# Kernel tuning notes

Hardware: AMD Instinct MI355X
Metric: run time of the kernel (lower is better)

## Reference

```python
import jax, jax.numpy as jnp
import numpy as np

B, IN_DIM, C, E, TOPK = 16384, 768, 50, 8, 2
RH = 256          # router hidden_dim
HS = [512, 256]   # expert hidden_sizes
THR = 0.05        # BitNet-1.58b ternarization threshold


def _xavier(k, shape):
    fan_out, fan_in = shape[-2], shape[-1]
    lim = float(np.sqrt(6.0 / (fan_in + fan_out)))
    return jax.random.uniform(k, shape, jnp.float32, -lim, lim)


def setup_inputs() -> dict:
    key = jax.random.key(0)
    ks = jax.random.split(key, 8)
    return {
        "x": jax.random.normal(ks[0], (B, IN_DIM), jnp.float32),
        # Router MLP: in_dim -> RH -> RH//2 -> E (torch Linear: W is (out,in))
        "rW1": _xavier(ks[1], (RH, IN_DIM)), "rb1": jnp.zeros((RH,), jnp.float32),
        "rW2": _xavier(ks[2], (RH // 2, RH)), "rb2": jnp.zeros((RH // 2,), jnp.float32),
        "rW3": _xavier(ks[3], (E, RH // 2)), "rb3": jnp.zeros((E,), jnp.float32),
        # Stacked expert weights: (E, out, in)
        "eW1": _xavier(ks[4], (E, HS[0], IN_DIM)), "eb1": jnp.zeros((E, HS[0]), jnp.float32),
        "eW2": _xavier(ks[5], (E, HS[1], HS[0])), "eb2": jnp.zeros((E, HS[1]), jnp.float32),
        "eW3": _xavier(ks[6], (E, C, HS[1])), "eb3": jnp.zeros((E, C), jnp.float32),
    }


def _ternary(W):
    # BitNet-1.58b: ternarize weights with |w|>threshold, scale by mean |W| per matrix
    scale = jnp.mean(jnp.abs(W), axis=(-2, -1), keepdims=True)
    Wq = jnp.sign(W) * (jnp.abs(W) > THR).astype(W.dtype)
    return Wq * scale


def reference(x, rW1, rb1, rW2, rb2, rW3, rb3, eW1, eb1, eW2, eb2, eW3, eb3):
    # ---- Router (eval mode: dropout = identity) ----
    h = jax.nn.relu(x @ rW1.T + rb1)
    h = jax.nn.relu(h @ rW2.T + rb2)
    router_logits = h @ rW3.T + rb3                      # (B, E)
    router_p = jax.nn.softmax(router_logits, axis=1)     # (B, E)

    # ---- Top-k gating; scatter gate weights back to dense (B, E) ----
    k_val, k_idx = jax.lax.top_k(router_p, TOPK)         # (B, K)
    rows = jnp.arange(x.shape[0])[:, None]
    gate = jnp.zeros_like(router_p).at[rows, k_idx].set(k_val)  # 0 for unselected experts

    # ---- Batched ternary-quantized expert MLPs (all experts, all samples) ----
    W1q, W2q, W3q = _ternary(eW1), _ternary(eW2), _ternary(eW3)
    a1 = jax.nn.relu(jnp.einsum('bd,ehd->ebh', x, W1q) + eb1[:, None, :])   # (E,B,H1)
    a2 = jax.nn.relu(jnp.einsum('ebh,egh->ebg', a1, W2q) + eb2[:, None, :]) # (E,B,H2)
    expert_logits = jnp.einsum('ebg,ecg->ebc', a2, W3q) + eb3[:, None, :]   # (E,B,C)

    # ---- Weighted combine over top-k experts (equivalent to the per-expert loop) ----
    out = jnp.einsum('ebc,be->bc', expert_logits, gate) / TOPK              # (B,C)

    lb_loss = jnp.float32(0.0)  # eval mode: self.training is False
    return (out, router_p, lb_loss)
```

## Files before the change

kernel.cpp:

```cpp
#include <hip/hip_runtime.h>
#include <hip/hip_bf16.h>

typedef __attribute__((ext_vector_type(4))) float f32x4;
typedef __attribute__((ext_vector_type(8))) short bf16x8;

#define B_ROWS 16384
#define IN_DIM 768
#define H1 512
#define H2 256
#define NC 50
#define NE 8
#define RH1 256
#define RH2 128
#define CHK 128

static __device__ __forceinline__ f32x4 mfma16(bf16x8 a, bf16x8 b, f32x4 c) {
    return __builtin_amdgcn_mfma_f32_16x16x32_bf16(a, b, c, 0, 0, 0);
}

static __device__ __forceinline__ bf16x8 expand_frag(uint2 pw) {
    unsigned q0 = (pw.x & 0x01010101u) << 7;
    unsigned q1 = (pw.y & 0x01010101u) << 7;
    union { unsigned u[4]; bf16x8 v; } r;
    r.u[0] = __builtin_amdgcn_perm(pw.x, q0, 0x05010400u);
    r.u[1] = __builtin_amdgcn_perm(pw.x, q0, 0x07030602u);
    r.u[2] = __builtin_amdgcn_perm(pw.y, q1, 0x05010400u);
    r.u[3] = __builtin_amdgcn_perm(pw.y, q1, 0x07030602u);
    return r.v;
}

static __device__ __forceinline__ void decomp_f4(float4 v, ushort4* hv, ushort4* lv) {
    float vv[4] = {v.x, v.y, v.z, v.w};
    ushort ho[4], lo4[4];
    #pragma unroll
    for (int q = 0; q < 4; ++q) {
        __hip_bfloat16 h = __float2bfloat16(vv[q]);
        float hf = __bfloat162float(h);
        __hip_bfloat16 l = __float2bfloat16(vv[q] - hf);
        ho[q] = *(ushort*)&h; lo4[q] = *(ushort*)&l;
    }
    *hv = make_ushort4(ho[0], ho[1], ho[2], ho[3]);
    *lv = make_ushort4(lo4[0], lo4[1], lo4[2], lo4[3]);
}

__global__ __launch_bounds__(512) void pack_absum_kernel(
    const float* __restrict__ eW1, const float* __restrict__ eW2, const float* __restrict__ eW3,
    unsigned char* __restrict__ W1p8, unsigned char* __restrict__ W2p8,
    unsigned char* __restrict__ W3p8,
    float* __restrict__ p1, float* __restrict__ p2, float* __restrict__ p3,
    const float* __restrict__ rW1, ushort* __restrict__ rw1hp, ushort* __restrict__ rw1lp,
    const float* __restrict__ rW2, ushort* __restrict__ rw2hp, ushort* __restrict__ rw2lp,
    int* __restrict__ counts)
{
    if (blockIdx.y == 24) {
        int u = blockIdx.x * 512 + threadIdx.x;
        const float* src; ushort* dh; ushort* dl;
        if (u < 24576) {
            int lane = u & 63, nblk = (u >> 6) & 15, ks = u >> 10;
            int n = nblk * 16 + (lane & 15), k = ks * 32 + (lane >> 4) * 8;
            src = rW1 + (size_t)n * IN_DIM + k;
            dh = rw1hp + (size_t)u * 8; dl = rw1lp + (size_t)u * 8;
        } else {
            int v = u - 24576;
            if (v >= 4096) return;
            int lane = v & 63, nblk = (v >> 6) & 7, ks = v >> 9;
            int n = nblk * 16 + (lane & 15), k = ks * 32 + (lane >> 4) * 8;
            src = rW2 + (size_t)n * RH1 + k;
            dh = rw2hp + (size_t)v * 8; dl = rw2lp + (size_t)v * 8;
        }
        ushort oh[8], ol[8];
        #pragma unroll
        for (int j = 0; j < 8; ++j) {
            float w = src[j];
            __hip_bfloat16 h = __float2bfloat16(w);
            float hf = __bfloat162float(h);
            __hip_bfloat16 l = __float2bfloat16(w - hf);
            oh[j] = *(ushort*)&h; ol[j] = *(ushort*)&l;
        }
        ((ushort4*)dh)[0] = make_ushort4(oh[0], oh[1], oh[2], oh[3]);
        ((ushort4*)dh)[1] = make_ushort4(oh[4], oh[5], oh[6], oh[7]);
        ((ushort4*)dl)[0] = make_ushort4(ol[0], ol[1], ol[2], ol[3]);
        ((ushort4*)dl)[1] = make_ushort4(ol[4], ol[5], ol[6], ol[7]);
        return;
    }

    const int mat = blockIdx.y >> 3, e = blockIdx.y & 7;
    const int u = blockIdx.x * 512 + threadIdx.x;
    if (blockIdx.x == 0 && blockIdx.y == 0 && threadIdx.x < 8) counts[threadIdx.x] = 0;
    const float* src; unsigned char* dst; int valid = 1; float* P; int np;
    if (mat == 0) {
        int lane = u & 63, nblk = (u >> 6) & 31, ks = u >> 11;
        int n = nblk * 16 + (lane & 15), k = ks * 32 + (lane >> 4) * 8;
        src = eW1 + ((size_t)e * H1 + n) * IN_DIM + k;
        dst = W1p8 + (size_t)e * 393216
            + (size_t)ks * 16384 + (nblk >> 1) * 1024 + lane * 16 + (nblk & 1) * 8;
        P = p1; np = 96;
    } else if (mat == 1) {
        int lane = u & 63, nblk = (u >> 6) & 15, ks = u >> 10;
        if (u >= 16384) {
            float s = 0.f;
            const int lane2 = threadIdx.x & 63, wave2 = threadIdx.x >> 6;
            #pragma unroll
            for (int o = 32; o; o >>= 1) s += __shfl_down(s, o);
            __shared__ float redp[8];
            if (lane2 == 0) redp[wave2] = s;
            __syncthreads();
            return;
        }
        int n = nblk * 16 + (lane & 15), k = ks * 32 + (lane >> 4) * 8;
        src = eW2 + ((size_t)e * H2 + n) * H1 + k;
        dst = W2p8 + (size_t)e * 131072
            + (size_t)ks * 8192 + (nblk >> 1) * 1024 + lane * 16 + (nblk & 1) * 8;
        P = p2; np = 32;
    } else {
        if (u >= 2048) {
            float s = 0.f;
            const int lane2 = threadIdx.x & 63, wave2 = threadIdx.x >> 6;
            #pragma unroll
            for (int o = 32; o; o >>= 1) s += __shfl_down(s, o);
            __shared__ float redp2[8];
            if (lane2 == 0) redp2[wave2] = s;
            __syncthreads();
            return;
        }
        int lane = u & 63, nblk = (u >> 6) & 3, ks = u >> 8;
        int n = nblk * 16 + (lane & 15), k = ks * 32 + (lane >> 4) * 8;
        valid = (n < NC);
        src = eW3 + ((size_t)e * NC + (valid ? n : 0)) * H2 + k;
        dst = W3p8 + ((size_t)e * 2048 + u) * 8;
        P = p3; np = 4;
    }
    unsigned lo = 0, hi = 0;
    float s = 0.f;
    #pragma unroll
    for (int j = 0; j < 4; ++j) {
        float w = valid ? src[j] : 0.f;
        s += fabsf(w);
        unsigned c = (fabsf(w) > 0.05f) ? (w > 0.f ? 0x3Fu : 0xBFu) : 0u;
        lo |= c << (8 * j);
    }
    #pragma unroll
    for (int j = 0; j < 4; ++j) {
        float w = valid ? src[4 + j] : 0.f;
        s += fabsf(w);
        unsigned c = (fabsf(w) > 0.05f) ? (w > 0.f ? 0x3Fu : 0xBFu) : 0u;
        hi |= c << (8 * j);
    }
    *(uint2*)dst = make_uint2(lo, hi);
    const int lane = threadIdx.x & 63, wave = threadIdx.x >> 6;
    #pragma unroll
    for (int o = 32; o; o >>= 1) s += __shfl_down(s, o);
    __shared__ float red[8];
    if (lane == 0) red[wave] = s;
    __syncthreads();
    if (threadIdx.x == 0) {
        float t = 0.f;
        #pragma unroll
        for (int i = 0; i < 8; ++i) t += red[i];
        P[e * np + blockIdx.x] = t;
    }
}

__global__ __launch_bounds__(1024) void router_fused_kernel(
    const float* __restrict__ x, ushort* __restrict__ xh_out,
    const ushort* __restrict__ rw1hp, const ushort* __restrict__ rw1lp, const float* __restrict__ rb1,
    const ushort* __restrict__ rw2hp, const ushort* __restrict__ rw2lp, const float* __restrict__ rb2,
    const float* __restrict__ rW3, const float* __restrict__ rb3,
    float* __restrict__ router_p, float* __restrict__ gate,
    float* __restrict__ lb_out, int* __restrict__ t2)
{
    __shared__ __align__(16) unsigned char smem[68608];
    ushort (*Xdh)[32][136] = (ushort(*)[32][136])(smem);
    ushort (*Xdl)[32][136] = (ushort(*)[32][136])(smem + 17408);
    ushort (*h1hs)[264]    = (ushort(*)[264])(smem + 34816);
    ushort (*h1ls)[264]    = (ushort(*)[264])(smem + 51712);
    float (*h2s)[132]      = (float(*)[132])(smem);

    const int tid = threadIdx.x, wave = tid >> 6, lane = tid & 63;
    const int lm = lane & 15, lk = lane >> 4;
    const int r0 = blockIdx.x * 32;

    const int srow = tid >> 5;
    const int sc4r = (tid & 31) * 4;
    const float* sg = x + (size_t)(r0 + srow) * IN_DIM + sc4r;
    ushort* xo = xh_out + (size_t)(r0 + srow) * IN_DIM + sc4r;

    {
        float4 sv = *(const float4*)sg;
        ushort4 hv, lv;
        decomp_f4(sv, &hv, &lv);
        *(ushort4*)&Xdh[0][srow][sc4r] = hv;
        *(ushort4*)&Xdl[0][srow][sc4r] = lv;
        *(ushort4*)xo = hv;
    }
    __syncthreads();

    {
        f32x4 acc[2] = {};
        const ushort* wph = rw1hp + (size_t)(wave * 64 + lane) * 8;
        const ushort* wpl = rw1lp + (size_t)(wave * 64 + lane) * 8;
        uint4 ph[4], pl[4];
        #pragma unroll
        for (int k = 0; k < 4; ++k) {
            ph[k] = *(const uint4*)(wph + (size_t)k * 8192);
            pl[k] = *(const uint4*)(wpl + (size_t)k * 8192);
        }
        for (int i = 0; i < 6; ++i) {
            float4 sv;
            if (i + 1 < 6) sv = *(const float4*)(sg + (i + 1) * CHK);
            const ushort (*Xch)[136] = Xdh[i & 1];
            const ushort (*Xcl)[136] = Xdl[i & 1];
            #pragma unroll
            for (int k4 = 0; k4 < 4; ++k4) {
                uint4 ch = ph[k4], cl = pl[k4];
                if (i + 1 < 6) {
                    ph[k4] = *(const uint4*)(wph + (size_t)(4 * i + 4 + k4) * 8192);
                    pl[k4] = *(const uint4*)(wpl + (size_t)(4 * i + 4 + k4) * 8192);
                }
                const int ko = k4 * 32 + lk * 8;
                bf16x8 ah0 = *(const bf16x8*)&Xch[lm][ko];
                bf16x8 al0 = *(const bf16x8*)&Xcl[lm][ko];
                bf16x8 ah1 = *(const bf16x8*)&Xch[16 + lm][ko];
                bf16x8 al1 = *(const bf16x8*)&Xcl[16 + lm][ko];
                bf16x8 bh = *(bf16x8*)&ch;
                bf16x8 bl = *(bf16x8*)&cl;
                acc[0] = mfma16(ah0, bh, acc[0]);
                acc[0] = mfma16(ah0, bl, acc[0]);
                acc[0] = mfma16(al0, bh, acc[0]);
                acc[1] = mfma16(ah1, bh, acc[1]);
                acc[1] = mfma16(ah1, bl, acc[1]);
                acc[1] = mfma16(al1, bh, acc[1]);
            }
            if (i + 1 < 6) {
                ushort4 hv, lv;
                decomp_f4(sv, &hv, &lv);
                *(ushort4*)&Xdh[(i + 1) & 1][srow][sc4r] = hv;
                *(ushort4*)&Xdl[(i + 1) & 1][srow][sc4r] = lv;
                *(ushort4*)(xo + (i + 1) * CHK) = hv;
            }
            __syncthreads();
        }
        int col = wave * 16 + lm;
        float bv = rb1[col];
        #pragma unroll
        for (int m = 0; m < 2; ++m)
            #pragma unroll
            for (int r = 0; r < 4; ++r) {
                float v = acc[m][r] + bv;
                v = v > 0.f ? v : 0.f;
                __hip_bfloat16 h = __float2bfloat16(v);
                float hf = __bfloat162float(h);
                __hip_bfloat16 l = __float2bfloat16(v - hf);
                int row = m * 16 + lk * 4 + r;
                h1hs[row][col] = *(ushort*)&h;
                h1ls[row][col] = *(ushort*)&l;
            }
    }
    __syncthreads();

    {
        const int mt = wave >> 3, nb = wave & 7;
        const ushort* w2h = rw2hp + (size_t)(nb * 64 + lane) * 8;
        const ushort* w2l = rw2lp + (size_t)(nb * 64 + lane) * 8;
        f32x4 acc2 = {};
        uint4 pha = *(const uint4*)(w2h);
        uint4 pla = *(const uint4*)(w2l);
        uint4 phb = *(const uint4*)(w2h + 4096);
        uint4 plb = *(const uint4*)(w2l + 4096);
        for (int s = 0; s < 8; s += 2) {
            uint4 cha = pha, cla = pla, chb = phb, clb = plb;
            if (s + 2 < 8) {
                pha = *(const uint4*)(w2h + (size_t)(s + 2) * 4096);
                pla = *(const uint4*)(w2l + (size_t)(s + 2) * 4096);
                phb = *(const uint4*)(w2h + (size_t)(s + 3) * 4096);
                plb = *(const uint4*)(w2l + (size_t)(s + 3) * 4096);
            }
            {
                const int ko = s * 32 + lk * 8;
                bf16x8 ah = *(const bf16x8*)&h1hs[mt * 16 + lm][ko];
                bf16x8 al = *(const bf16x8*)&h1ls[mt * 16 + lm][ko];
                bf16x8 bh = *(bf16x8*)&cha;
                bf16x8 bl = *(bf16x8*)&cla;
                acc2 = mfma16(ah, bh, acc2);
                acc2 = mfma16(ah, bl, acc2);
                acc2 = mfma16(al, bh, acc2);
            }
            {
                const int ko = (s + 1) * 32 + lk * 8;
                bf16x8 ah = *(const bf16x8*)&h1hs[mt * 16 + lm][ko];
                bf16x8 al = *(const bf16x8*)&h1ls[mt * 16 + lm][ko];
                bf16x8 bh = *(bf16x8*)&chb;
                bf16x8 bl = *(bf16x8*)&clb;
                acc2 = mfma16(ah, bh, acc2);
                acc2 = mfma16(ah, bl, acc2);
                acc2 = mfma16(al, bh, acc2);
            }
        }
        __syncthreads();
        int col2 = nb * 16 + lm;
        float bv = rb2[col2];
        #pragma unroll
        for (int r = 0; r < 4; ++r) {
            float v = acc2[r] + bv;
            h2s[mt * 16 + lk * 4 + r][col2] = v > 0.f ? v : 0.f;
        }
    }
    __syncthreads();

    const int o = lane >> 3, kq = lane & 7;
    #pragma unroll
    for (int i = 0; i < 2; ++i) {
        int rloc = wave * 2 + i;
        int b = r0 + rloc;
        float s = 0.f;
        #pragma unroll
        for (int q = 0; q < 4; ++q) {
            float4 hv = *(const float4*)&h2s[rloc][kq * 16 + q * 4];
            float4 wv = *(const float4*)&rW3[o * RH2 + kq * 16 + q * 4];
            s += hv.x * wv.x + hv.y * wv.y + hv.z * wv.z + hv.w * wv.w;
        }
        s += __shfl_xor(s, 1);
        s += __shfl_xor(s, 2);
        s += __shfl_xor(s, 4);
        float logit = s + rb3[o];
        float l[8];
        #pragma unroll
        for (int j = 0; j < 8; ++j) l[j] = __shfl(logit, j * 8);
        float m = l[0];
        #pragma unroll
        for (int j = 1; j < 8; ++j) m = fmaxf(m, l[j]);
        float p[8]; float sum = 0.f;
        #pragma unroll
        for (int j = 0; j < 8; ++j) { p[j] = expf(l[j] - m); sum += p[j]; }
        float inv = 1.f / sum;
        #pragma unroll
        for (int j = 0; j < 8; ++j) p[j] *= inv;
        int i1 = 0; float v1 = p[0];
        #pragma unroll
        for (int j = 1; j < 8; ++j) if (p[j] > v1) { v1 = p[j]; i1 = j; }
        int i2 = -1; float v2 = -1.f;
        #pragma unroll
        for (int j = 0; j < 8; ++j) if (j != i1 && p[j] > v2) { v2 = p[j]; i2 = j; }
        if (lane < 8) {
            router_p[(size_t)b * 8 + lane] = p[lane];
            float gv = (lane == i1) ? v1 * 0.5f : ((lane == i2) ? v2 * 0.5f : 0.f);
            gate[(size_t)b * 8 + lane] = gv;
        }
        if (lane == 0) t2[b] = i1 | (i2 << 8);
    }
    if (blockIdx.x == 0 && tid == 0) lb_out[0] = 0.f;
}

__global__ __launch_bounds__(256) void build_lists_kernel(
    const int* __restrict__ t2, int* __restrict__ counts, int* __restrict__ ent,
    const float* __restrict__ p1, const float* __restrict__ p2, const float* __restrict__ p3,
    float* __restrict__ s1, float* __restrict__ s2, float* __restrict__ s3)
{
    if (blockIdx.x == 0 && threadIdx.x < 24) {
        int t = threadIdx.x;
        if (t < 8) {
            float a = 0.f;
            for (int i = 0; i < 96; ++i) a += p1[t * 96 + i];
            s1[t] = a / (float)(H1 * IN_DIM);
        } else if (t < 16) {
            int e = t - 8; float a = 0.f;
            for (int i = 0; i < 32; ++i) a += p2[e * 32 + i];
            s2[e] = a / (float)(H2 * H1);
        } else {
            int e = t - 16; float a = 0.f;
            for (int i = 0; i < 4; ++i) a += p3[e * 4 + i];
            s3[e] = a / (float)(NC * H2);
        }
    }
    __shared__ int hist[8], base[8];
    const int r = blockIdx.x * 256 + threadIdx.x;
    if (threadIdx.x < 8) hist[threadIdx.x] = 0;
    __syncthreads();
    const int v = t2[r];
    const int i1 = v & 255, i2 = v >> 8;
    const int rk1 = atomicAdd(&hist[i1], 1);
    const int rk2 = atomicAdd(&hist[i2], 1);
    __syncthreads();
    if (threadIdx.x < 8) base[threadIdx.x] = atomicAdd(&counts[threadIdx.x], hist[threadIdx.x]);
    __syncthreads();
    ent[i1 * B_ROWS + base[i1] + rk1] = (r << 1);
    ent[i2 * B_ROWS + base[i2] + rk2] = (r << 1) | 1;
}

__global__ __launch_bounds__(1024) void expert_fused_kernel(
    const ushort* __restrict__ xh,
    const unsigned char* __restrict__ W1p8, const unsigned char* __restrict__ W2p8,
    const unsigned char* __restrict__ W3p8,
    const float* __restrict__ s1, const float* __restrict__ s2, const float* __restrict__ s3,
    const float* __restrict__ eb1, const float* __restrict__ eb2, const float* __restrict__ eb3,
    const float* __restrict__ gate,
    const int* __restrict__ counts, const int* __restrict__ ent,
    float* __restrict__ S0, float* __restrict__ S1)
{
    int pfx[9]; pfx[0] = 0;
    #pragma unroll
    for (int i = 0; i < 8; ++i) pfx[i + 1] = pfx[i] + ((counts[i] + 63) >> 6);
    const int T = pfx[8];
    const int R = (T + 7) >> 3;
    const int xcd = blockIdx.x & 7, j = blockIdx.x >> 3;
    if (j >= R) return;
    const int g = xcd * R + j;
    if (g >= T) return;
    int e = 0;
    #pragma unroll
    for (int i = 0; i < 7; ++i) if (g >= pfx[i + 1]) e = i + 1;
    const int t = g - pfx[e];
    const int cnt = counts[e];

    __shared__ __align__(16) unsigned char smem[101376];
    __hip_bfloat16 (*A1s)[520] = (__hip_bfloat16(*)[520])(smem);
    __hip_bfloat16 (*A2s)[264] = (__hip_bfloat16(*)[264])(smem + 66560);
    ushort (*Xd)[64][136]      = (ushort(*)[64][136])(smem + 66560);
    __shared__ int rowL[64];
    __shared__ int slotL[64];
    __shared__ float gL[64];

    const int tid = threadIdx.x;
    const int wave = tid >> 6;
    const int lane = tid & 63;
    const int lm = lane & 15;
    const int lk = lane >> 4;

    if (tid < 64) {
        int idx = t * 64 + tid;
        if (idx < cnt) {
            int entv = ent[e * B_ROWS + idx];
            int r = entv >> 1;
            rowL[tid] = r;
            slotL[tid] = entv & 1;
            gL[tid] = gate[(size_t)r * NE + e];
        } else {
            rowL[tid] = -1; slotL[tid] = 0; gL[tid] = 0.f;
        }
    }
    __syncthreads();

    const int srow = tid >> 4;
    const int sc8  = (tid & 15) * 8;
    int SR = rowL[srow]; if (SR < 0) SR = 0;
    const ushort* sg = xh + (size_t)SR * IN_DIM + sc8;
    const unsigned char* Wsrc1 = W1p8 + (size_t)e * 393216;
    const unsigned char* Wsrc2 = W2p8 + (size_t)e * 131072;
    const unsigned char* Wsrc3 = W3p8 + (size_t)e * 16384;

    {
        bf16x8 sv = *(const bf16x8*)sg;
        *(bf16x8*)&Xd[0][srow][sc8] = sv;
    }
    __syncthreads();

    {
        f32x4 acc[4][2] = {};
        const int w2 = wave * 2;
        const unsigned char* wp1 = Wsrc1 + wave * 1024 + lane * 16;
        uint4 pw[4];
        #pragma unroll
        for (int k = 0; k < 4; ++k)
            pw[k] = *(const uint4*)(wp1 + (size_t)k * 16384);
        for (int i = 0; i < 6; ++i) {
            bf16x8 sv;
            if (i + 1 < 6) sv = *(const bf16x8*)(sg + (i + 1) * CHK);
            uint4 cur[4];
            #pragma unroll
            for (int k = 0; k < 4; ++k) cur[k] = pw[k];
            if (i + 1 < 6) {
                #pragma unroll
                for (int k = 0; k < 4; ++k)
                    pw[k] = *(const uint4*)(wp1 + (size_t)(4 * i + 4 + k) * 16384);
            }
            const ushort (*Xc)[136] = Xd[i & 1];
            #pragma unroll
            for (int k4 = 0; k4 < 4; ++k4) {
                const int ko = k4 * 32 + lk * 8;
                bf16x8 a0 = *(const bf16x8*)&Xc[     lm][ko];
                bf16x8 a1 = *(const bf16x8*)&Xc[16 + lm][ko];
                bf16x8 a2 = *(const bf16x8*)&Xc[32 + lm][ko];
                bf16x8 a3 = *(const bf16x8*)&Xc[48 + lm][ko];
                bf16x8 b0 = expand_frag(make_uint2(cur[k4].x, cur[k4].y));
                bf16x8 b1 = expand_frag(make_uint2(cur[k4].z, cur[k4].w));
                acc[0][0] = mfma16(a0, b0, acc[0][0]);
                acc[1][0] = mfma16(a1, b0, acc[1][0]);
                acc[2][0] = mfma16(a2, b0, acc[2][0]);
                acc[3][0] = mfma16(a3, b0, acc[3][0]);
                acc[0][1] = mfma16(a0, b1, acc[0][1]);
                acc[1][1] = mfma16(a1, b1, acc[1][1]);
                acc[2][1] = mfma16(a2, b1, acc[2][1]);
                acc[3][1] = mfma16(a3, b1, acc[3][1]);
            }
            if (i + 1 < 6) *(bf16x8*)&Xd[(i + 1) & 1][srow][sc8] = sv;
            __syncthreads();
        }
        const float* bias = eb1 + e * H1;
        const float sc = s1[e];
        #pragma unroll
        for (int n = 0; n < 2; ++n) {
            int ncol = (w2 + n) * 16 + lm;
            float bv = bias[ncol];
            #pragma unroll
            for (int m = 0; m < 4; ++m)
                #pragma unroll
                for (int r = 0; r < 4; ++r) {
                    float v = fmaf(acc[m][n][r], sc, bv);
                    v = v > 0.f ? v : 0.f;
                    A1s[m * 16 + lk * 4 + r][ncol] = __float2bfloat16(v);
                }
        }
    }
    __syncthreads();

    {
        const int mt = wave >> 3, ntw = wave & 7;
        const unsigned char* wp2 = Wsrc2 + ntw * 1024 + lane * 16;
        f32x4 acc[2][2] = {};
        uint4 pwa = *(const uint4*)(wp2);
        uint4 pwb = *(const uint4*)(wp2 + 8192);
        for (int s = 0; s < 16; s += 2) {
            uint4 c0 = pwa, c1 = pwb;
            if (s + 2 < 16) {
                pwa = *(const uint4*)(wp2 + (size_t)(s + 2) * 8192);
                pwb = *(const uint4*)(wp2 + (size_t)(s + 3) * 8192);
            }
            {
                const int ko = s * 32 + lk * 8;
                bf16x8 a0 = *(const bf16x8*)&A1s[mt * 32 +      lm][ko];
                bf16x8 a1 = *(const bf16x8*)&A1s[mt * 32 + 16 + lm][ko];
                bf16x8 b0 = expand_frag(make_uint2(c0.x, c0.y));
                bf16x8 b1 = expand_frag(make_uint2(c0.z, c0.w));
                acc[0][0] = mfma16(a0, b0, acc[0][0]);
                acc[1][0] = mfma16(a1, b0, acc[1][0]);
                acc[0][1] = mfma16(a0, b1, acc[0][1]);
                acc[1][1] = mfma16(a1, b1, acc[1][1]);
            }
            {
                const int ko = (s + 1) * 32 + lk * 8;
                bf16x8 a0 = *(const bf16x8*)&A1s[mt * 32 +      lm][ko];
                bf16x8 a1 = *(const bf16x8*)&A1s[mt * 32 + 16 + lm][ko];
                bf16x8 b0 = expand_frag(make_uint2(c1.x, c1.y));
                bf16x8 b1 = expand_frag(make_uint2(c1.z, c1.w));
                acc[0][0] = mfma16(a0, b0, acc[0][0]);
                acc[1][0] = mfma16(a1, b0, acc[1][0]);
                acc[0][1] = mfma16(a0, b1, acc[0][1]);
                acc[1][1] = mfma16(a1, b1, acc[1][1]);
            }
        }
        const float* bias = eb2 + e * H2;
        const float sc = s2[e];
        #pragma unroll
        for (int n = 0; n < 2; ++n) {
            int ncol = (ntw * 2 + n) * 16 + lm;
            float bv = bias[ncol];
            #pragma unroll
            for (int m = 0; m < 2; ++m)
                #pragma unroll
                for (int r = 0; r < 4; ++r) {
                    float v = fmaf(acc[m][n][r], sc, bv);
                    v = v > 0.f ? v : 0.f;
                    A2s[mt * 32 + m * 16 + lk * 4 + r][ncol] = __float2bfloat16(v);
                }
        }
    }
    __syncthreads();

    {
        const int mt = wave & 3, nt = wave >> 2;
        f32x4 acc = {};
        #pragma unroll
        for (int s = 0; s < 8; ++s) {
            bf16x8 a = *(const bf16x8*)&A2s[mt * 16 + lm][s * 32 + lk * 8];
            uint2 pw = *(const uint2*)(Wsrc3 + ((s * 4 + nt) * 64 + lane) * 8);
            bf16x8 b = expand_frag(pw);
            acc = mfma16(a, b, acc);
        }
        int col = nt * 16 + lm;
        if (col < NC) {
            const float bv = eb3[e * NC + col];
            const float sc = s3[e];
            #pragma unroll
            for (int r = 0; r < 4; ++r) {
                int row = mt * 16 + lk * 4 + r;
                int R2 = rowL[row];
                if (R2 >= 0) {
                    float v = gL[row] * fmaf(acc[r], sc, bv);
                    float* Sb = slotL[row] ? S1 : S0;
                    Sb[(size_t)R2 * 64 + col] = v;
                }
            }
        }
    }
}

__global__ __launch_bounds__(256) void combine_kernel(
    const float* __restrict__ S0, const float* __restrict__ S1, float* __restrict__ out)
{
    int i = blockIdx.x * 256 + threadIdx.x;
    if (i < B_ROWS * NC) {
        int row = i / NC, col = i % NC;
        out[i] = S0[(size_t)row * 64 + col] + S1[(size_t)row * 64 + col];
    }
}

extern "C" void kernel_launch(void* const* d_in, const int* in_sizes, int n_in,
                              void* d_out, int out_size, void* d_ws, size_t ws_size,
                              hipStream_t stream) {
    const float* x   = (const float*)d_in[0];
    const float* rW1 = (const float*)d_in[1];
    const float* rb1 = (const float*)d_in[2];
    const float* rW2 = (const float*)d_in[3];
    const float* rb2 = (const float*)d_in[4];
    const float* rW3 = (const float*)d_in[5];
    const float* rb3 = (const float*)d_in[6];
    const float* eW1 = (const float*)d_in[7];
    const float* eb1 = (const float*)d_in[8];
    const float* eW2 = (const float*)d_in[9];
    const float* eb2 = (const float*)d_in[10];
    const float* eW3 = (const float*)d_in[11];
    const float* eb3 = (const float*)d_in[12];

    float* out_main = (float*)d_out;
    float* router_p = out_main + (size_t)B_ROWS * NC;
    float* lb_out   = router_p + (size_t)B_ROWS * NE;

    char* ws = (char*)d_ws;
    size_t off = 0;
    unsigned char* W1p8 = (unsigned char*)(ws + off); off += (size_t)NE * 49152 * 8;
    unsigned char* W2p8 = (unsigned char*)(ws + off); off += (size_t)NE * 16384 * 8;
    unsigned char* W3p8 = (unsigned char*)(ws + off); off += (size_t)NE * 2048 * 8;
    ushort* xh  = (ushort*)(ws + off); off += (size_t)B_ROWS * IN_DIM * 2;
    float* S0   = (float*)(ws + off);  off += (size_t)B_ROWS * 64 * 4;
    float* S1   = (float*)(ws + off);  off += (size_t)B_ROWS * 64 * 4;
    ushort* rw1hp = (ushort*)(ws + off); off += (size_t)24576 * 8 * 2;
    ushort* rw1lp = (ushort*)(ws + off); off += (size_t)24576 * 8 * 2;
    ushort* rw2hp = (ushort*)(ws + off); off += (size_t)4096 * 8 * 2;
    ushort* rw2lp = (ushort*)(ws + off); off += (size_t)4096 * 8 * 2;
    float* gate = (float*)(ws + off);  off += (size_t)B_ROWS * NE * 4;
    int*   ent  = (int*)(ws + off);    off += (size_t)NE * B_ROWS * 4;
    int*   t2   = (int*)(ws + off);    off += (size_t)B_ROWS * 4;
    int* counts = (int*)(ws + off);    off += 256;
    float* s1   = (float*)(ws + off);  off += 256;
    float* s2   = (float*)(ws + off);  off += 256;
    float* s3   = (float*)(ws + off);  off += 256;
    float* p1   = (float*)(ws + off);  off += NE * 96 * 4;
    float* p2   = (float*)(ws + off);  off += NE * 32 * 4;
    float* p3   = (float*)(ws + off);  off += NE * 4 * 4;

    pack_absum_kernel<<<dim3(96, 25), 512, 0, stream>>>(
        eW1, eW2, eW3, W1p8, W2p8, W3p8, p1, p2, p3,
        rW1, rw1hp, rw1lp, rW2, rw2hp, rw2lp, counts);

    router_fused_kernel<<<B_ROWS / 32, 1024, 0, stream>>>(
        x, xh, rw1hp, rw1lp, rb1, rw2hp, rw2lp, rb2, rW3, rb3, router_p, gate, lb_out, t2);
    build_lists_kernel<<<B_ROWS / 256, 256, 0, stream>>>(
        t2, counts, ent, p1, p2, p3, s1, s2, s3);

    expert_fused_kernel<<<1024, 1024, 0, stream>>>(
        xh, W1p8, W2p8, W3p8, s1, s2, s3, eb1, eb2, eb3, gate, counts, ent, S0, S1);
    combine_kernel<<<(B_ROWS * NC + 255) / 256, 256, 0, stream>>>(S0, S1, out_main);
}
```

Before: 119.1 us.

## Retile expert GEMM warp tiles and fuse combine via atomic adds

Layer 1 switches each wave from a 64x32 tile to a 32x64 tile, and layer 2 from 32x32 to 16x64. This changes the balance between A reads from shared memory and ternary B-fragment expansion per MFMA. The two per-slot scratch buffers and the combine kernel are removed: the layer-3 results are atomically added straight into the output, which is zeroed by a memset first. This drops one kernel launch and the round trip through the scratch buffers, at the cost of float atomics, and the sum order of the two experts is no longer fixed.

```diff
diff --git a/kernel.cpp b/kernel.cpp
--- a/kernel.cpp
+++ b/kernel.cpp
@@ -395,7 +395,7 @@
     const float* __restrict__ eb1, const float* __restrict__ eb2, const float* __restrict__ eb3,
     const float* __restrict__ gate,
     const int* __restrict__ counts, const int* __restrict__ ent,
-    float* __restrict__ S0, float* __restrict__ S1)
+    float* __restrict__ out)
 {
     int pfx[9]; pfx[0] = 0;
     #pragma unroll
@@ -455,104 +455,56 @@
     __syncthreads();
 
     {
-        f32x4 acc[4][2] = {};
-        const int w2 = wave * 2;
-        const unsigned char* wp1 = Wsrc1 + wave * 1024 + lane * 16;
-        uint4 pw[4];
-        #pragma unroll
-        for (int k = 0; k < 4; ++k)
-            pw[k] = *(const uint4*)(wp1 + (size_t)k * 16384);
+        f32x4 acc[2][4] = {};
+        const int mt2 = wave >> 3;
+        const int nb4 = wave & 7;
+        const unsigned char* wp1 = Wsrc1 + nb4 * 2048 + lane * 16;
+        uint4 pw[4][2];
+        #pragma unroll
+        for (int k = 0; k < 4; ++k) {
+            pw[k][0] = *(const uint4*)(wp1 + (size_t)k * 16384);
+            pw[k][1] = *(const uint4*)(wp1 + (size_t)k * 16384 + 1024);
+        }
         for (int i = 0; i < 6; ++i) {
             bf16x8 sv;
             if (i + 1 < 6) sv = *(const bf16x8*)(sg + (i + 1) * CHK);
-            uint4 cur[4];
-            #pragma unroll
-            for (int k = 0; k < 4; ++k) cur[k] = pw[k];
+            uint4 cur[4][2];
+            #pragma unroll
+            for (int k = 0; k < 4; ++k) { cur[k][0] = pw[k][0]; cur[k][1] = pw[k][1]; }
             if (i + 1 < 6) {
                 #pragma unroll
-                for (int k = 0; k < 4; ++k)
-                    pw[k] = *(const uint4*)(wp1 + (size_t)(4 * i + 4 + k) * 16384);
+                for (int k = 0; k < 4; ++k) {
+                    pw[k][0] = *(const uint4*)(wp1 + (size_t)(4 * i + 4 + k) * 16384);
+                    pw[k][1] = *(const uint4*)(wp1 + (size_t)(4 * i + 4 + k) * 16384 + 1024);
+                }
             }
             const ushort (*Xc)[136] = Xd[i & 1];
             #pragma unroll
             for (int k4 = 0; k4 < 4; ++k4) {
                 const int ko = k4 * 32 + lk * 8;
-                bf16x8 a0 = *(const bf16x8*)&Xc[     lm][ko];
-                bf16x8 a1 = *(const bf16x8*)&Xc[16 + lm][ko];
-                bf16x8 a2 = *(const bf16x8*)&Xc[32 + lm][ko];
-                bf16x8 a3 = *(const bf16x8*)&Xc[48 + lm][ko];
-                bf16x8 b0 = expand_frag(make_uint2(cur[k4].x, cur[k4].y));
-                bf16x8 b1 = expand_frag(make_uint2(cur[k4].z, cur[k4].w));
-                acc[0][0] = mfma16(a0, b0, acc[0][0]);
-                acc[1][0] = mfma16(a1, b0, acc[1][0]);
-                acc[2][0] = mfma16(a2, b0, acc[2][0]);
-                acc[3][0] = mfma16(a3, b0, acc[3][0]);
-                acc[0][1] = mfma16(a0, b1, acc[0][1]);
-                acc[1][1] = mfma16(a1, b1, acc[1][1]);
-                acc[2][1] = mfma16(a2, b1, acc[2][1]);
-                acc[3][1] = mfma16(a3, b1, acc[3][1]);
-            }
-            if (i + 1 < 6) *(bf16x8*)&Xd[(i + 1) & 1][srow][sc8] = sv;
-            __syncthreads();
-        }
-        const float* bias = eb1 + e * H1;
-        const float sc = s1[e];
-        #pragma unroll
-        for (int n = 0; n < 2; ++n) {
-            int ncol = (w2 + n) * 16 + lm;
-            float bv = bias[ncol];
-            #pragma unroll
-            for (int m = 0; m < 4; ++m)
-                #pragma unroll
-                for (int r = 0; r < 4; ++r) {
-                    float v = fmaf(acc[m][n][r], sc, bv);
-                    v = v > 0.f ? v : 0.f;
-                    A1s[m * 16 + lk * 4 + r][ncol] = __float2bfloat16(v);
-                }
-        }
-    }
-    __syncthreads();
-
-    {
-        const int mt = wave >> 3, ntw = wave & 7;
-        const unsigned char* wp2 = Wsrc2 + ntw * 1024 + lane * 16;
-        f32x4 acc[2][2] = {};
-        uint4 pwa = *(const uint4*)(wp2);
-        uint4 pwb = *(const uint4*)(wp2 + 8192);
-        for (int s = 0; s < 16; s += 2) {
-            uint4 c0 = pwa, c1 = pwb;
-            if (s + 2 < 16) {
-                pwa = *(const uint4*)(wp2 + (size_t)(s + 2) * 8192);
-                pwb = *(const uint4*)(wp2 + (size_t)(s + 3) * 8192);
-            }
-            {
-                const int ko = s * 32 + lk * 8;
-                bf16x8 a0 = *(const bf16x8*)&A1s[mt * 32 +      lm][ko];
-                bf16x8 a1 = *(const bf16x8*)&A1s[mt * 32 + 16 + lm][ko];
-                bf16x8 b0 = expand_frag(make_uint2(c0.x, c0.y));
-                bf16x8 b1 = expand_frag(make_uint2(c0.z, c0.w));
+                bf16x8 a0 = *(const bf16x8*)&Xc[mt2 * 32 +      lm][ko];
+                bf16x8 a1 = *(const bf16x8*)&Xc[mt2 * 32 + 16 + lm][ko];
+                bf16x8 b0 = expand_frag(make_uint2(cur[k4][0].x, cur[k4][0].y));
+                bf16x8 b1 = expand_frag(make_uint2(cur[k4][0].z, cur[k4][0].w));
+                bf16x8 b2 = expand_frag(make_uint2(cur[k4][1].x, cur[k4][1].y));
+                bf16x8 b3 = expand_frag(make_uint2(cur[k4][1].z, cur[k4][1].w));
                 acc[0][0] = mfma16(a0, b0, acc[0][0]);
                 acc[1][0] = mfma16(a1, b0, acc[1][0]);
                 acc[0][1] = mfma16(a0, b1, acc[0][1]);
                 acc[1][1] = mfma16(a1, b1, acc[1][1]);
-            }
-            {
-                const int ko = (s + 1) * 32 + lk * 8;
-                bf16x8 a0 = *(const bf16x8*)&A1s[mt * 32 +      lm][ko];
-                bf16x8 a1 = *(const bf16x8*)&A1s[mt * 32 + 16 + lm][ko];
-                bf16x8 b0 = expand_frag(make_uint2(c1.x, c1.y));
-                bf16x8 b1 = expand_frag(make_uint2(c1.z, c1.w));
-                acc[0][0] = mfma16(a0, b0, acc[0][0]);
-                acc[1][0] = mfma16(a1, b0, acc[1][0]);
-                acc[0][1] = mfma16(a0, b1, acc[0][1]);
-                acc[1][1] = mfma16(a1, b1, acc[1][1]);
-            }
-        }
-        const float* bias = eb2 + e * H2;
-        const float sc = s2[e];
-        #pragma unroll
-        for (int n = 0; n < 2; ++n) {
-            int ncol = (ntw * 2 + n) * 16 + lm;
+                acc[0][2] = mfma16(a0, b2, acc[0][2]);
+                acc[1][2] = mfma16(a1, b2, acc[1][2]);
+                acc[0][3] = mfma16(a0, b3, acc[0][3]);
+                acc[1][3] = mfma16(a1, b3, acc[1][3]);
+            }
+            if (i + 1 < 6) *(bf16x8*)&Xd[(i + 1) & 1][srow][sc8] = sv;
+            __syncthreads();
+        }
+        const float* bias = eb1 + e * H1;
+        const float sc = s1[e];
+        #pragma unroll
+        for (int n = 0; n < 4; ++n) {
+            int ncol = (nb4 * 4 + n) * 16 + lm;
             float bv = bias[ncol];
             #pragma unroll
             for (int m = 0; m < 2; ++m)
@@ -560,8 +512,68 @@
                 for (int r = 0; r < 4; ++r) {
                     float v = fmaf(acc[m][n][r], sc, bv);
                     v = v > 0.f ? v : 0.f;
-                    A2s[mt * 32 + m * 16 + lk * 4 + r][ncol] = __float2bfloat16(v);
+                    A1s[mt2 * 32 + m * 16 + lk * 4 + r][ncol] = __float2bfloat16(v);
                 }
+        }
+    }
+    __syncthreads();
+
+    {
+        const int mt = wave & 3;
+        const int ng = wave >> 2;
+        const unsigned char* wp2 = Wsrc2 + ng * 2048 + lane * 16;
+        f32x4 acc[4] = {};
+        uint4 pwa[2], pwb[2];
+        pwa[0] = *(const uint4*)(wp2);
+        pwa[1] = *(const uint4*)(wp2 + 1024);
+        pwb[0] = *(const uint4*)(wp2 + 8192);
+        pwb[1] = *(const uint4*)(wp2 + 8192 + 1024);
+        for (int s = 0; s < 16; s += 2) {
+            uint4 c0[2], c1[2];
+            c0[0] = pwa[0]; c0[1] = pwa[1]; c1[0] = pwb[0]; c1[1] = pwb[1];
+            if (s + 2 < 16) {
+                pwa[0] = *(const uint4*)(wp2 + (size_t)(s + 2) * 8192);
+                pwa[1] = *(const uint4*)(wp2 + (size_t)(s + 2) * 8192 + 1024);
+                pwb[0] = *(const uint4*)(wp2 + (size_t)(s + 3) * 8192);
+                pwb[1] = *(const uint4*)(wp2 + (size_t)(s + 3) * 8192 + 1024);
+            }
+            {
+                const int ko = s * 32 + lk * 8;
+                bf16x8 a = *(const bf16x8*)&A1s[mt * 16 + lm][ko];
+                bf16x8 b0 = expand_frag(make_uint2(c0[0].x, c0[0].y));
+                bf16x8 b1 = expand_frag(make_uint2(c0[0].z, c0[0].w));
+                bf16x8 b2 = expand_frag(make_uint2(c0[1].x, c0[1].y));
+                bf16x8 b3 = expand_frag(make_uint2(c0[1].z, c0[1].w));
+                acc[0] = mfma16(a, b0, acc[0]);
+                acc[1] = mfma16(a, b1, acc[1]);
+                acc[2] = mfma16(a, b2, acc[2]);
+                acc[3] = mfma16(a, b3, acc[3]);
+            }
+            {
+                const int ko = (s + 1) * 32 + lk * 8;
+                bf16x8 a = *(const bf16x8*)&A1s[mt * 16 + lm][ko];
+                bf16x8 b0 = expand_frag(make_uint2(c1[0].x, c1[0].y));
+                bf16x8 b1 = expand_frag(make_uint2(c1[0].z, c1[0].w));
+                bf16x8 b2 = expand_frag(make_uint2(c1[1].x, c1[1].y));
+                bf16x8 b3 = expand_frag(make_uint2(c1[1].z, c1[1].w));
+                acc[0] = mfma16(a, b0, acc[0]);
+                acc[1] = mfma16(a, b1, acc[1]);
+                acc[2] = mfma16(a, b2, acc[2]);
+                acc[3] = mfma16(a, b3, acc[3]);
+            }
+        }
+        const float* bias = eb2 + e * H2;
+        const float sc = s2[e];
+        #pragma unroll
+        for (int n = 0; n < 4; ++n) {
+            int ncol = (ng * 4 + n) * 16 + lm;
+            float bv = bias[ncol];
+            #pragma unroll
+            for (int r = 0; r < 4; ++r) {
+                float v = fmaf(acc[n][r], sc, bv);
+                v = v > 0.f ? v : 0.f;
+                A2s[mt * 16 + lk * 4 + r][ncol] = __float2bfloat16(v);
+            }
         }
     }
     __syncthreads();
@@ -586,21 +598,10 @@
                 int R2 = rowL[row];
                 if (R2 >= 0) {
                     float v = gL[row] * fmaf(acc[r], sc, bv);
-                    float* Sb = slotL[row] ? S1 : S0;
-                    Sb[(size_t)R2 * 64 + col] = v;
+                    atomicAdd(&out[(size_t)R2 * NC + col], v);
                 }
             }
         }
-    }
-}
-
-__global__ __launch_bounds__(256) void combine_kernel(
-    const float* __restrict__ S0, const float* __restrict__ S1, float* __restrict__ out)
-{
-    int i = blockIdx.x * 256 + threadIdx.x;
-    if (i < B_ROWS * NC) {
-        int row = i / NC, col = i % NC;
-        out[i] = S0[(size_t)row * 64 + col] + S1[(size_t)row * 64 + col];
     }
 }
 
@@ -631,8 +632,6 @@
     unsigned char* W2p8 = (unsigned char*)(ws + off); off += (size_t)NE * 16384 * 8;
     unsigned char* W3p8 = (unsigned char*)(ws + off); off += (size_t)NE * 2048 * 8;
     ushort* xh  = (ushort*)(ws + off); off += (size_t)B_ROWS * IN_DIM * 2;
-    float* S0   = (float*)(ws + off);  off += (size_t)B_ROWS * 64 * 4;
-    float* S1   = (float*)(ws + off);  off += (size_t)B_ROWS * 64 * 4;
     ushort* rw1hp = (ushort*)(ws + off); off += (size_t)24576 * 8 * 2;
     ushort* rw1lp = (ushort*)(ws + off); off += (size_t)24576 * 8 * 2;
     ushort* rw2hp = (ushort*)(ws + off); off += (size_t)4096 * 8 * 2;
@@ -648,6 +647,8 @@
     float* p2   = (float*)(ws + off);  off += NE * 32 * 4;
     float* p3   = (float*)(ws + off);  off += NE * 4 * 4;
 
+    hipMemsetAsync(out_main, 0, (size_t)B_ROWS * NC * sizeof(float), stream);
+
     pack_absum_kernel<<<dim3(96, 25), 512, 0, stream>>>(
         eW1, eW2, eW3, W1p8, W2p8, W3p8, p1, p2, p3,
         rW1, rw1hp, rw1lp, rW2, rw2hp, rw2lp, counts);
@@ -658,6 +659,5 @@
         t2, counts, ent, p1, p2, p3, s1, s2, s3);
 
     expert_fused_kernel<<<1024, 1024, 0, stream>>>(
-        xh, W1p8, W2p8, W3p8, s1, s2, s3, eb1, eb2, eb3, gate, counts, ent, S0, S1);
-    combine_kernel<<<(B_ROWS * NC + 255) / 256, 256, 0, stream>>>(S0, S1, out_main);
-}
+        xh, W1p8, W2p8, W3p8, s1, s2, s3, eb1, eb2, eb3, gate, counts, ent, out_main);
+}
```

Result: slower. 138.8 us (+16.6%).
